# Kernel optimization log

Hardware: AMD Instinct MI355X
Metric: run time of the kernel (lower is better)

The kernel has to match this reference:

```python
import jax, jax.numpy as jnp
import numpy as np

N_NODES = 100000
N_EDGES = 3200000
N_GRAPHS = 256
HIDDEN = 64
F_IN = 9
GRAPH_INPUTS = 4


def setup_inputs() -> dict:
    key = jax.random.key(0)
    ks = jax.random.split(key, 20)
    x = jax.random.normal(ks[0], (N_NODES, F_IN), dtype=jnp.float32)
    edge_index = jax.random.randint(ks[1], (2, N_EDGES), 0, N_NODES)
    batch = jnp.sort(jax.random.randint(ks[2], (N_NODES,), 0, N_GRAPHS))
    batch = batch.at[0].set(0).at[-1].set(N_GRAPHS - 1)
    u = jax.random.normal(ks[3], (N_GRAPHS, GRAPH_INPUTS), dtype=jnp.float32)

    def lin(k, fi, fo):
        k1, k2 = jax.random.split(k)
        s = 1.0 / np.sqrt(fi)
        W = jax.random.uniform(k1, (fi, fo), minval=-s, maxval=s, dtype=jnp.float32)
        b = jax.random.uniform(k2, (fo,), minval=-s, maxval=s, dtype=jnp.float32)
        return W, b

    W1, b1 = lin(ks[4], F_IN, HIDDEN)
    W2, b2 = lin(ks[5], HIDDEN, HIDDEN)
    W3, b3 = lin(ks[6], HIDDEN, HIDDEN)
    A1, c1 = lin(ks[7], HIDDEN + GRAPH_INPUTS, 50)
    A2, c2 = lin(ks[8], 50, 30)
    A3, c3 = lin(ks[9], 30, 20)
    A4, c4 = lin(ks[10], 20, 5)
    A5, c5 = lin(ks[11], 5, 1)
    return dict(x=x, edge_index=edge_index, batch=batch, u=u,
                W1=W1, b1=b1, W2=W2, b2=b2, W3=W3, b3=b3,
                A1=A1, c1=c1, A2=A2, c2=c2, A3=A3, c3=c3,
                A4=A4, c4=c4, A5=A5, c5=c5)


def reference(x, edge_index, batch, u,
              W1, b1, W2, b2, W3, b3,
              A1, c1, A2, c2, A3, c3, A4, c4, A5, c5):
    N = x.shape[0]
    loops = jnp.arange(N, dtype=edge_index.dtype)
    src = jnp.concatenate([edge_index[0], loops])  # self-loops appended (PyG GCNConv default)
    dst = jnp.concatenate([edge_index[1], loops])
    deg = jax.ops.segment_sum(jnp.ones_like(dst, dtype=x.dtype), dst, num_segments=N)
    dinv = jax.lax.rsqrt(jnp.maximum(deg, 1.0))  # deg >= 1 due to self-loops
    norm = dinv[src] * dinv[dst]  # symmetric normalization

    def conv(h, W, b):
        h = h @ W
        msg = h[src] * norm[:, None]          # gather + scale
        return jax.ops.segment_sum(msg, dst, num_segments=N) + b  # scatter-add

    h = jax.nn.relu(conv(x, W1, b1))
    h = jax.nn.relu(conv(h, W2, b2))
    h = jax.nn.relu(conv(h, W3, b3))

    G = u.shape[0]
    sums = jax.ops.segment_sum(h, batch, num_segments=G)
    cnt = jax.ops.segment_sum(jnp.ones((N,), x.dtype), batch, num_segments=G)
    pooled = sums / jnp.maximum(cnt, 1.0)[:, None]  # global_mean_pool
    # dropout p=0.2 is identity at inference (training=False)
    z = jnp.concatenate([pooled, u], axis=1)
    z = jax.nn.relu(z @ A1 + c1)
    z = jax.nn.relu(z @ A2 + c2)
    z = jax.nn.relu(z @ A3 + c3)
    z = jax.nn.relu(z @ A4 + c4)
    z = jax.nn.relu(z @ A5 + c5)
    return z
```

## Files before the change

### kernel.cpp

```cpp
#include <hip/hip_runtime.h>

#define H 64
#define BNODE_SHIFT 8
#define BNODES 256
#define CHUNK 4096
#define EPT 16

static __device__ __forceinline__ float b2f(ushort b) {
    return __uint_as_float(((unsigned int)b) << 16);
}
static __device__ __forceinline__ ushort f2b(float f) {
    unsigned int u = __float_as_uint(f);
    return (ushort)((u + 0x7FFF + ((u >> 16) & 1)) >> 16);
}
#define RFL(x) __builtin_amdgcn_readfirstlane(x)

#if __has_builtin(__builtin_amdgcn_cvt_f32_fp8) && __has_builtin(__builtin_amdgcn_cvt_pk_fp8_f32)
#define HWFP8 1
#else
#define HWFP8 0
#endif

static __device__ __forceinline__ float fp8d(unsigned int b) {
#if HWFP8
    return __builtin_amdgcn_cvt_f32_fp8((int)b, 0);
#else
    unsigned em = b & 0x7F;
    float mag = (em >= 8) ? __uint_as_float((em << 20) + 0x3C000000u)
                          : (float)em * 0.001953125f;
    return (b & 0x80) ? -mag : mag;
#endif
}
static __device__ __forceinline__ unsigned char fp8e(float f) {
#if HWFP8
    return (unsigned char)(__builtin_amdgcn_cvt_pk_fp8_f32(f, f, 0, false) & 0xFF);
#else
    unsigned u = __float_as_uint(f);
    unsigned s = (u >> 24) & 0x80;
    float af = fabsf(f);
    if (af >= 448.f) return (unsigned char)(s | 0x7E);
    if (af < 0.0009765625f) return (unsigned char)s;
    if (af < 0.015625f) {
        int m = (int)rintf(af * 512.f);
        if (m > 7) return (unsigned char)(s | 0x08);
        return (unsigned char)(s | m);
    }
    int e; float fr = frexpf(af, &e);
    int q = (int)rintf(fr * 16.f);
    if (q == 16) { q = 8; e += 1; }
    int E = e + 6;
    if (E > 15 || (E == 15 && (q & 7) > 6)) return (unsigned char)(s | 0x7E);
    return (unsigned char)(s | (E << 3) | (q & 7));
#endif
}

__global__ void zero_i32(int* p, int n) {
    int i = blockIdx.x * blockDim.x + threadIdx.x;
    if (i < n) p[i] = 0;
}

__global__ void bucket_hist(const int* __restrict__ dst, int E,
                            int* __restrict__ bcounts, int nbuck) {
    __shared__ int hist[512];
    for (int i = threadIdx.x; i < nbuck; i += blockDim.x) hist[i] = 0;
    __syncthreads();
    for (int e = blockIdx.x * blockDim.x + threadIdx.x; e < E; e += gridDim.x * blockDim.x)
        atomicAdd(&hist[dst[e] >> BNODE_SHIFT], 1);
    __syncthreads();
    for (int i = threadIdx.x; i < nbuck; i += blockDim.x) {
        int v = hist[i];
        if (v) atomicAdd(&bcounts[i], v);
    }
}

__global__ void bucket_scan(const int* __restrict__ bcounts, int* __restrict__ boff,
                            int* __restrict__ bcur, int* __restrict__ rowstart,
                            int nbuck, int E, int N) {
    __shared__ int t[1024];
    int tid = threadIdx.x;
    int v = (tid < nbuck) ? bcounts[tid] : 0;
    t[tid] = v;
    __syncthreads();
    for (int off = 1; off < 1024; off <<= 1) {
        int x = (tid >= off) ? t[tid - off] : 0;
        __syncthreads();
        t[tid] += x;
        __syncthreads();
    }
    if (tid < nbuck) {
        int o = t[tid] - v;
        boff[tid] = o;
        bcur[tid * 16] = o;
    }
    if (tid == 0) { boff[nbuck] = E; rowstart[N] = E; }
}

__global__ void edge_sort_scatter(const int* __restrict__ src, const int* __restrict__ dst,
                                  int E, int nbuck,
                                  int* __restrict__ bcur, int* __restrict__ pairs4) {
    __shared__ int hist[392];
    __shared__ int bstart[393];
    __shared__ int cur[392];
    __shared__ int gbase[392];
    __shared__ int wsum[256];
    __shared__ int packed[CHUNK];
    __shared__ int gpos[CHUNK];

    int t = threadIdx.x;
    int chunkBase = blockIdx.x * CHUNK;

    int dreg[EPT], sreg[EPT];
    for (int i = t; i < nbuck; i += 256) hist[i] = 0;
    __syncthreads();
#pragma unroll
    for (int k = 0; k < EPT; ++k) {
        int e = chunkBase + t + k * 256;
        dreg[k] = (e < E) ? dst[e] : -1;
        sreg[k] = (e < E) ? src[e] : 0;
    }
#pragma unroll
    for (int k = 0; k < EPT; ++k)
        if (dreg[k] >= 0) atomicAdd(&hist[dreg[k] >> BNODE_SHIFT], 1);
    __syncthreads();

    int a0 = (2 * t < nbuck) ? hist[2 * t] : 0;
    int a1 = (2 * t + 1 < nbuck) ? hist[2 * t + 1] : 0;
    int s2 = a0 + a1;
    wsum[t] = s2;
    __syncthreads();
    for (int off = 1; off < 256; off <<= 1) {
        int x = (t >= off) ? wsum[t - off] : 0;
        __syncthreads();
        wsum[t] += x;
        __syncthreads();
    }
    int base = wsum[t] - s2;
    if (2 * t < nbuck)     bstart[2 * t] = base;
    if (2 * t + 1 < nbuck) bstart[2 * t + 1] = base + a0;
    if (t == 255) bstart[nbuck] = wsum[255];
    __syncthreads();

    for (int b = t; b < nbuck; b += 256) {
        int cnt = bstart[b + 1] - bstart[b];
        gbase[b] = cnt ? (atomicAdd(&bcur[b * 16], cnt) - bstart[b]) : 0;
        cur[b] = bstart[b];
    }
    __syncthreads();

#pragma unroll
    for (int k = 0; k < EPT; ++k) {
        if (dreg[k] >= 0) {
            int d = dreg[k];
            int b = d >> BNODE_SHIFT;
            int pos = atomicAdd(&cur[b], 1);
            packed[pos] = sreg[k] | ((d & (BNODES - 1)) << 20);
            gpos[pos] = gbase[b] + pos;
        }
    }
    __syncthreads();

    int nloc = bstart[nbuck];
    for (int j = t; j < nloc; j += 256)
        pairs4[gpos[j]] = packed[j];
}

__global__ void bucket_build(const int* __restrict__ pairs4, const int* __restrict__ boff,
                             int* __restrict__ col, int* __restrict__ rowstart,
                             float* __restrict__ dinv, int N) {
    __shared__ int hist[BNODES];
    __shared__ int cur[BNODES];
    int b = blockIdx.x;
    int lo = boff[b], hi = boff[b + 1];
    int node0 = b << BNODE_SHIFT;
    int tid = threadIdx.x;
    hist[tid] = 0;
    __syncthreads();
    for (int e = lo + tid; e < hi; e += 256)
        atomicAdd(&hist[(pairs4[e] >> 20) & (BNODES - 1)], 1);
    __syncthreads();
    int v = hist[tid];
    cur[tid] = v;
    __syncthreads();
    for (int off = 1; off < BNODES; off <<= 1) {
        int x = (tid >= off) ? cur[tid - off] : 0;
        __syncthreads();
        cur[tid] += x;
        __syncthreads();
    }
    {
        int ex = cur[tid] - v;
        int node = node0 + tid;
        if (node < N) {
            rowstart[node] = lo + ex;
            dinv[node] = rsqrtf((float)(v + 1));
        }
        cur[tid] = ex;
    }
    __syncthreads();
    for (int e = lo + tid; e < hi; e += 256) {
        int pr = pairs4[e];
        int p = atomicAdd(&cur[(pr >> 20) & (BNODES - 1)], 1);
        col[lo + p] = pr & 0xFFFFF;
    }
}

__global__ void graph_bounds(const int* __restrict__ batch, int* __restrict__ nodestart,
                             int N, int G) {
    int i = blockIdx.x * blockDim.x + threadIdx.x;
    if (i >= N) return;
    int b = batch[i];
    int bp = (i == 0) ? -1 : batch[i - 1];
    for (int g = bp + 1; g <= b; ++g) nodestart[g] = i;
    if (i == N - 1) nodestart[G] = N;
}

__global__ void pool_mean(const ushort* __restrict__ h, const int* __restrict__ nodestart,
                          float* __restrict__ pooled, int G) {
    int g = blockIdx.x;
    int lo = nodestart[g], hi = nodestart[g + 1];
    int f = threadIdx.x & 63, w = threadIdx.x >> 6;
    float acc = 0.f;
    for (int n = lo + w; n < hi; n += 4) acc += b2f(h[(size_t)n * H + f]);
    __shared__ float red[4][64];
    red[w][f] = acc;
    __syncthreads();
    if (w == 0) {
        float s = red[0][f] + red[1][f] + red[2][f] + red[3][f];
        float c = (float)(hi - lo);
        pooled[g * H + f] = s / fmaxf(c, 1.f);
    }
}

__global__ void prep_x8(const float* __restrict__ x, const float* __restrict__ dinv,
                        unsigned char* __restrict__ xb, int N) {
    int i = blockIdx.x * blockDim.x + threadIdx.x;
    if (i >= N * 16) return;
    int n = i >> 4, k = i & 15;
    xb[i] = (k < 9) ? fp8e(x[n * 9 + k] * dinv[n]) : (unsigned char)0;
}

__global__ void conv1_fused(const unsigned char* __restrict__ xb, const float* __restrict__ dinv,
                            const int* __restrict__ rowstart,
                            const int* __restrict__ col, const float* __restrict__ W1,
                            const float* __restrict__ b1, ushort* __restrict__ out, int N) {
    int gtid = blockIdx.x * blockDim.x + threadIdx.x;
    int i = RFL(gtid >> 6);
    int lane = threadIdx.x & 63;
    int f16 = lane & 15, grp = lane >> 4;
    if (i >= N) return;
    float di = dinv[i];
    float sv = fp8d(xb[(size_t)i * 16 + f16]);
    float acc = 0.f;
    int s = rowstart[i], e = rowstart[i + 1];
    for (int base = s; base < e; base += 64) {
        int cnt = e - base;
        if (cnt > 64) cnt = 64;
        int idx = 0;
        if (lane < cnt) idx = col[base + lane];
        for (int j = 0; j < cnt; j += 8) {
            int j0 = j + grp, j1 = j + 4 + grp;
            int s0 = __shfl(idx, j0);
            int s1 = __shfl(idx, j1 & 63);
            float v0 = (j0 < cnt) ? fp8d(xb[(size_t)s0 * 16 + f16]) : 0.f;
            float v1 = (j1 < cnt) ? fp8d(xb[(size_t)s1 * 16 + f16]) : 0.f;
            acc += v0 + v1;
        }
    }
    acc += __shfl_xor(acc, 16);
    acc += __shfl_xor(acc, 32);
    float aggf = di * (acc + sv);

    float o = b1[lane];
#pragma unroll
    for (int k = 0; k < 9; ++k) {
        float ak = __shfl(aggf, k);
        o = fmaf(ak, W1[k * H + lane], o);
    }
    out[(size_t)i * H + lane] = f2b(fmaxf(o, 0.f));
}

__global__ void lin_h(const ushort* __restrict__ h, const float* __restrict__ W,
                      const float* __restrict__ dinv, unsigned char* __restrict__ out, int N) {
    __shared__ float Ws[H * H];
    __shared__ float hs[32 * H];
    int tid = threadIdx.x;
    int node0 = blockIdx.x * 32;
    for (int idx = tid; idx < H * H; idx += 256) Ws[idx] = W[idx];
    for (int idx = tid; idx < 32 * H; idx += 256) {
        int n = node0 + (idx >> 6);
        hs[idx] = (n < N) ? b2f(h[(size_t)n * H + (idx & 63)]) : 0.f;
    }
    __syncthreads();
    int nlb = tid >> 6, f = tid & 63;
    float a[8];
#pragma unroll
    for (int j = 0; j < 8; ++j) a[j] = 0.f;
#pragma unroll 8
    for (int k = 0; k < H; ++k) {
        float w = Ws[k * H + f];
#pragma unroll
        for (int j = 0; j < 8; ++j)
            a[j] = fmaf(hs[(nlb + 4 * j) * H + k], w, a[j]);
    }
#pragma unroll
    for (int j = 0; j < 8; ++j) {
        int n = node0 + nlb + 4 * j;
        if (n < N) out[(size_t)n * H + f] = fp8e(a[j] * dinv[n]);
    }
}

__global__ void aggregate_8(const unsigned char* __restrict__ hb, const float* __restrict__ dinv,
                            const int* __restrict__ rowstart,
                            const int* __restrict__ col, const float* __restrict__ bias,
                            ushort* __restrict__ out, int N) {
    int gtid = blockIdx.x * blockDim.x + threadIdx.x;
    int i = RFL(gtid >> 6);
    int f = threadIdx.x & 63;
    if (i >= N) return;
    float acc = fp8d(hb[(size_t)i * H + f]);
    int s = rowstart[i], e = rowstart[i + 1];
    int p = s;
    for (; p + 16 <= e; p += 16) {
        int idx[16];
#pragma unroll
        for (int k = 0; k < 16; ++k) idx[k] = RFL(col[p + k]);
        float v[16];
#pragma unroll
        for (int k = 0; k < 16; ++k) v[k] = fp8d(hb[(size_t)idx[k] * H + f]);
        float s0 = ((v[0] + v[1]) + (v[2] + v[3])) + ((v[4] + v[5]) + (v[6] + v[7]));
        float s1 = ((v[8] + v[9]) + (v[10] + v[11])) + ((v[12] + v[13]) + (v[14] + v[15]));
        acc += s0 + s1;
    }
    for (; p + 4 <= e; p += 4) {
        int i0 = RFL(col[p + 0]);
        int i1 = RFL(col[p + 1]);
        int i2 = RFL(col[p + 2]);
        int i3 = RFL(col[p + 3]);
        float v0 = fp8d(hb[(size_t)i0 * H + f]);
        float v1 = fp8d(hb[(size_t)i1 * H + f]);
        float v2 = fp8d(hb[(size_t)i2 * H + f]);
        float v3 = fp8d(hb[(size_t)i3 * H + f]);
        acc += (v0 + v1) + (v2 + v3);
    }
    for (; p < e; ++p) {
        int s0 = RFL(col[p]);
        acc += fp8d(hb[(size_t)s0 * H + f]);
    }
    float r = fmaxf(bias[f] + dinv[i] * acc, 0.f);
    out[(size_t)i * H + f] = f2b(r);
}

__global__ void mlp(const float* __restrict__ pooled, const float* __restrict__ u,
                    const float* __restrict__ A1, const float* __restrict__ c1,
                    const float* __restrict__ A2, const float* __restrict__ c2,
                    const float* __restrict__ A3, const float* __restrict__ c3,
                    const float* __restrict__ A4, const float* __restrict__ c4,
                    const float* __restrict__ A5, const float* __restrict__ c5,
                    float* __restrict__ out, int G) {
    int wid = (blockIdx.x * blockDim.x + threadIdx.x) >> 6;
    int lane = threadIdx.x & 63;
    if (wid >= G) return;
    int g = wid;

    float zreg = pooled[g * H + lane];
    float u0 = u[g * 4 + 0], u1 = u[g * 4 + 1], u2 = u[g * 4 + 2], u3 = u[g * 4 + 3];

    float acc = (lane < 50) ? c1[lane] : 0.f;
#pragma unroll
    for (int k = 0; k < 64; ++k) {
        float zk = __shfl(zreg, k);
        float w = (lane < 50) ? A1[k * 50 + lane] : 0.f;
        acc = fmaf(zk, w, acc);
    }
    {
        float w;
        w = (lane < 50) ? A1[64 * 50 + lane] : 0.f; acc = fmaf(u0, w, acc);
        w = (lane < 50) ? A1[65 * 50 + lane] : 0.f; acc = fmaf(u1, w, acc);
        w = (lane < 50) ? A1[66 * 50 + lane] : 0.f; acc = fmaf(u2, w, acc);
        w = (lane < 50) ? A1[67 * 50 + lane] : 0.f; acc = fmaf(u3, w, acc);
    }
    float z1v = fmaxf(acc, 0.f);

    acc = (lane < 30) ? c2[lane] : 0.f;
#pragma unroll
    for (int k = 0; k < 50; ++k) {
        float zk = __shfl(z1v, k);
        float w = (lane < 30) ? A2[k * 30 + lane] : 0.f;
        acc = fmaf(zk, w, acc);
    }
    float z2v = fmaxf(acc, 0.f);

    acc = (lane < 20) ? c3[lane] : 0.f;
#pragma unroll
    for (int k = 0; k < 30; ++k) {
        float zk = __shfl(z2v, k);
        float w = (lane < 20) ? A3[k * 20 + lane] : 0.f;
        acc = fmaf(zk, w, acc);
    }
    float z3v = fmaxf(acc, 0.f);

    acc = (lane < 5) ? c4[lane] : 0.f;
#pragma unroll
    for (int k = 0; k < 20; ++k) {
        float zk = __shfl(z3v, k);
        float w = (lane < 5) ? A4[k * 5 + lane] : 0.f;
        acc = fmaf(zk, w, acc);
    }
    float z4v = fmaxf(acc, 0.f);

    acc = c5[0];
#pragma unroll
    for (int k = 0; k < 5; ++k) {
        float zk = __shfl(z4v, k);
        acc = fmaf(zk, A5[k], acc);
    }
    if (lane == 0) out[g] = fmaxf(acc, 0.f);
}

extern "C" void kernel_launch(void* const* d_in, const int* in_sizes, int n_in,
                              void* d_out, int out_size, void* d_ws, size_t ws_size,
                              hipStream_t stream) {
    const float* x     = (const float*)d_in[0];
    const int*   edge  = (const int*)d_in[1];
    const int*   batch = (const int*)d_in[2];
    const float* u     = (const float*)d_in[3];
    const float* W1 = (const float*)d_in[4];  const float* b1 = (const float*)d_in[5];
    const float* W2 = (const float*)d_in[6];  const float* b2 = (const float*)d_in[7];
    const float* W3 = (const float*)d_in[8];  const float* b3 = (const float*)d_in[9];
    const float* A1 = (const float*)d_in[10]; const float* c1 = (const float*)d_in[11];
    const float* A2 = (const float*)d_in[12]; const float* c2 = (const float*)d_in[13];
    const float* A3 = (const float*)d_in[14]; const float* c3 = (const float*)d_in[15];
    const float* A4 = (const float*)d_in[16]; const float* c4 = (const float*)d_in[17];
    const float* A5 = (const float*)d_in[18]; const float* c5 = (const float*)d_in[19];

    const int N = in_sizes[2];
    const int E = in_sizes[1] / 2;
    const int G = in_sizes[3] / 4;
    const int* src = edge;
    const int* dst = edge + E;
    const int nbuck = (N + BNODES - 1) >> BNODE_SHIFT;

    char* ws = (char*)d_ws;
    size_t off = 0;
    auto alloc = [&](size_t bytes) -> void* {
        void* p = ws + off;
        off = (off + bytes + 255) & ~(size_t)255;
        return p;
    };
    ushort*        hc  = (ushort*)alloc((size_t)N * H * 2);
    unsigned char* hb  = (unsigned char*)alloc((size_t)N * H);
    int*    col      = (int*)alloc((size_t)E * 4);
    unsigned char* xb = (unsigned char*)alloc((size_t)N * 16);
    int*    rowstart = (int*)alloc((size_t)(N + 1) * 4);
    float*  dinv     = (float*)alloc((size_t)N * 4);
    int*    bcounts  = (int*)alloc((size_t)nbuck * 4);
    int*    boff     = (int*)alloc((size_t)(nbuck + 1) * 4);
    int*    bcur     = (int*)alloc((size_t)nbuck * 64);
    int*    nodestart= (int*)alloc((size_t)(G + 1) * 4);
    float*  pooled   = (float*)alloc((size_t)G * H * 4);
    int*    pairs4   = (int*)hc;

    const int nbN   = (N + 255) / 256;
    const int nbAgg = (N + 3) / 4;
    const int nchunks = (E + CHUNK - 1) / CHUNK;

    zero_i32<<<(nbuck + 255) / 256, 256, 0, stream>>>(bcounts, nbuck);
    bucket_hist<<<256, 256, 0, stream>>>(dst, E, bcounts, nbuck);
    bucket_scan<<<1, 1024, 0, stream>>>(bcounts, boff, bcur, rowstart, nbuck, E, N);
    edge_sort_scatter<<<nchunks, 256, 0, stream>>>(src, dst, E, nbuck, bcur, pairs4);
    bucket_build<<<nbuck, 256, 0, stream>>>(pairs4, boff, col, rowstart, dinv, N);
    graph_bounds<<<nbN, 256, 0, stream>>>(batch, nodestart, N, G);

    prep_x8<<<(N * 16 + 255) / 256, 256, 0, stream>>>(x, dinv, xb, N);
    conv1_fused<<<nbAgg, 256, 0, stream>>>(xb, dinv, rowstart, col, W1, b1, hc, N);
    lin_h<<<(N + 31) / 32, 256, 0, stream>>>(hc, W2, dinv, hb, N);
    aggregate_8<<<nbAgg, 256, 0, stream>>>(hb, dinv, rowstart, col, b2, hc, N);
    lin_h<<<(N + 31) / 32, 256, 0, stream>>>(hc, W3, dinv, hb, N);
    aggregate_8<<<nbAgg, 256, 0, stream>>>(hb, dinv, rowstart, col, b3, hc, N);

    pool_mean<<<G, 256, 0, stream>>>(hc, nodestart, pooled, G);
    mlp<<<(G * 64 + 255) / 256, 256, 0, stream>>>(pooled, u, A1, c1, A2, c2, A3, c3,
                                                  A4, c4, A5, c5, (float*)d_out, G);
}
```

Measured before the change: 351.1 us.

## Fuse mean pooling into final aggregation via atomics and prefetch edge indices

The last GCN aggregation now atomically adds its ReLU outputs into per-graph float sums, and the mlp kernel divides by the node count. This removes the pool_mean kernel and the write and re-read of the final hidden features. The aggregation loop also prefetches the next 16 column indices before gathering the current ones, to hide index-load latency. The cost is heavy atomic contention, since all nodes of a graph target the same 64 addresses, and float summation order becomes nondeterministic.

```diff
diff --git a/kernel.cpp b/kernel.cpp
--- a/kernel.cpp
+++ b/kernel.cpp
@@ -58,6 +58,10 @@
     int i = blockIdx.x * blockDim.x + threadIdx.x;
     if (i < n) p[i] = 0;
 }
+__global__ void zero_f32(float* p, int n) {
+    int i = blockIdx.x * blockDim.x + threadIdx.x;
+    if (i < n) p[i] = 0.f;
+}
 
 __global__ void bucket_hist(const int* __restrict__ dst, int E,
                             int* __restrict__ bcounts, int nbuck) {
@@ -212,23 +216,6 @@
     int bp = (i == 0) ? -1 : batch[i - 1];
     for (int g = bp + 1; g <= b; ++g) nodestart[g] = i;
     if (i == N - 1) nodestart[G] = N;
-}
-
-__global__ void pool_mean(const ushort* __restrict__ h, const int* __restrict__ nodestart,
-                          float* __restrict__ pooled, int G) {
-    int g = blockIdx.x;
-    int lo = nodestart[g], hi = nodestart[g + 1];
-    int f = threadIdx.x & 63, w = threadIdx.x >> 6;
-    float acc = 0.f;
-    for (int n = lo + w; n < hi; n += 4) acc += b2f(h[(size_t)n * H + f]);
-    __shared__ float red[4][64];
-    red[w][f] = acc;
-    __syncthreads();
-    if (w == 0) {
-        float s = red[0][f] + red[1][f] + red[2][f] + red[3][f];
-        float c = (float)(hi - lo);
-        pooled[g * H + f] = s / fmaxf(c, 1.f);
-    }
 }
 
 __global__ void prep_x8(const float* __restrict__ x, const float* __restrict__ dinv,
@@ -309,10 +296,12 @@
     }
 }
 
+template <int MODE>
 __global__ void aggregate_8(const unsigned char* __restrict__ hb, const float* __restrict__ dinv,
                             const int* __restrict__ rowstart,
                             const int* __restrict__ col, const float* __restrict__ bias,
-                            ushort* __restrict__ out, int N) {
+                            ushort* __restrict__ out, float* __restrict__ pool,
+                            const int* __restrict__ batch, int N) {
     int gtid = blockIdx.x * blockDim.x + threadIdx.x;
     int i = RFL(gtid >> 6);
     int f = threadIdx.x & 63;
@@ -320,16 +309,28 @@
     float acc = fp8d(hb[(size_t)i * H + f]);
     int s = rowstart[i], e = rowstart[i + 1];
     int p = s;
-    for (; p + 16 <= e; p += 16) {
-        int idx[16];
-#pragma unroll
-        for (int k = 0; k < 16; ++k) idx[k] = RFL(col[p + k]);
-        float v[16];
-#pragma unroll
-        for (int k = 0; k < 16; ++k) v[k] = fp8d(hb[(size_t)idx[k] * H + f]);
-        float s0 = ((v[0] + v[1]) + (v[2] + v[3])) + ((v[4] + v[5]) + (v[6] + v[7]));
-        float s1 = ((v[8] + v[9]) + (v[10] + v[11])) + ((v[12] + v[13]) + (v[14] + v[15]));
-        acc += s0 + s1;
+    if (p + 16 <= e) {
+        int nxt[16];
+#pragma unroll
+        for (int k = 0; k < 16; ++k) nxt[k] = RFL(col[p + k]);
+        while (true) {
+            int idx[16];
+#pragma unroll
+            for (int k = 0; k < 16; ++k) idx[k] = nxt[k];
+            p += 16;
+            bool more = (p + 16 <= e);
+            if (more) {
+#pragma unroll
+                for (int k = 0; k < 16; ++k) nxt[k] = RFL(col[p + k]);
+            }
+            float v[16];
+#pragma unroll
+            for (int k = 0; k < 16; ++k) v[k] = fp8d(hb[(size_t)idx[k] * H + f]);
+            float s0 = ((v[0] + v[1]) + (v[2] + v[3])) + ((v[4] + v[5]) + (v[6] + v[7]));
+            float s1 = ((v[8] + v[9]) + (v[10] + v[11])) + ((v[12] + v[13]) + (v[14] + v[15]));
+            acc += s0 + s1;
+            if (!more) break;
+        }
     }
     for (; p + 4 <= e; p += 4) {
         int i0 = RFL(col[p + 0]);
@@ -347,10 +348,15 @@
         acc += fp8d(hb[(size_t)s0 * H + f]);
     }
     float r = fmaxf(bias[f] + dinv[i] * acc, 0.f);
-    out[(size_t)i * H + f] = f2b(r);
-}
-
-__global__ void mlp(const float* __restrict__ pooled, const float* __restrict__ u,
+    if (MODE == 0) {
+        out[(size_t)i * H + f] = f2b(r);
+    } else {
+        atomicAdd(&pool[(size_t)batch[i] * H + f], r);
+    }
+}
+
+__global__ void mlp(const float* __restrict__ pool, const int* __restrict__ nodestart,
+                    const float* __restrict__ u,
                     const float* __restrict__ A1, const float* __restrict__ c1,
                     const float* __restrict__ A2, const float* __restrict__ c2,
                     const float* __restrict__ A3, const float* __restrict__ c3,
@@ -362,7 +368,9 @@
     if (wid >= G) return;
     int g = wid;
 
-    float zreg = pooled[g * H + lane];
+    float cntf = (float)(nodestart[g + 1] - nodestart[g]);
+    float inv = 1.f / fmaxf(cntf, 1.f);
+    float zreg = pool[g * H + lane] * inv;
     float u0 = u[g * 4 + 0], u1 = u[g * 4 + 1], u2 = u[g * 4 + 2], u3 = u[g * 4 + 3];
 
     float acc = (lane < 50) ? c1[lane] : 0.f;
@@ -457,7 +465,7 @@
     int*    boff     = (int*)alloc((size_t)(nbuck + 1) * 4);
     int*    bcur     = (int*)alloc((size_t)nbuck * 64);
     int*    nodestart= (int*)alloc((size_t)(G + 1) * 4);
-    float*  pooled   = (float*)alloc((size_t)G * H * 4);
+    float*  pool     = (float*)alloc((size_t)G * H * 4);
     int*    pairs4   = (int*)hc;
 
     const int nbN   = (N + 255) / 256;
@@ -465,6 +473,7 @@
     const int nchunks = (E + CHUNK - 1) / CHUNK;
 
     zero_i32<<<(nbuck + 255) / 256, 256, 0, stream>>>(bcounts, nbuck);
+    zero_f32<<<(G * H + 255) / 256, 256, 0, stream>>>(pool, G * H);
     bucket_hist<<<256, 256, 0, stream>>>(dst, E, bcounts, nbuck);
     bucket_scan<<<1, 1024, 0, stream>>>(bcounts, boff, bcur, rowstart, nbuck, E, N);
     edge_sort_scatter<<<nchunks, 256, 0, stream>>>(src, dst, E, nbuck, bcur, pairs4);
@@ -474,11 +483,11 @@
     prep_x8<<<(N * 16 + 255) / 256, 256, 0, stream>>>(x, dinv, xb, N);
     conv1_fused<<<nbAgg, 256, 0, stream>>>(xb, dinv, rowstart, col, W1, b1, hc, N);
     lin_h<<<(N + 31) / 32, 256, 0, stream>>>(hc, W2, dinv, hb, N);
-    aggregate_8<<<nbAgg, 256, 0, stream>>>(hb, dinv, rowstart, col, b2, hc, N);
+    aggregate_8<0><<<nbAgg, 256, 0, stream>>>(hb, dinv, rowstart, col, b2, hc, nullptr, nullptr, N);
     lin_h<<<(N + 31) / 32, 256, 0, stream>>>(hc, W3, dinv, hb, N);
-    aggregate_8<<<nbAgg, 256, 0, stream>>>(hb, dinv, rowstart, col, b3, hc, N);
-
-    pool_mean<<<G, 256, 0, stream>>>(hc, nodestart, pooled, G);
-    mlp<<<(G * 64 + 255) / 256, 256, 0, stream>>>(pooled, u, A1, c1, A2, c2, A3, c3,
-                                                  A4, c4, A5, c5, (float*)d_out, G);
-}
+    aggregate_8<1><<<nbAgg, 256, 0, stream>>>(hb, dinv, rowstart, col, b3, nullptr, pool, batch, N);
+
+    mlp<<<(G * 64 + 255) / 256, 256, 0, stream>>>(pool, nodestart, u, A1, c1, A2, c2,
+                                                  A3, c3, A4, c4, A5, c5,
+                                                  (float*)d_out, G);
+}
```

Result: no change. 354.8 us (+1.1%).
